# Optimization experiments

Hardware: AMD Instinct MI355X
Metric: run time of the kernel (lower is better)

The kernel has to match this reference:

```python
import jax, jax.numpy as jnp
import numpy as np

B, S, K, N, G = 4, 2048, 4096, 11008, 128  # batch, seq, in_features, out_features, groupsize


def setup_inputs() -> dict:
    key = jax.random.key(0)
    k1, k2, k3, k4 = jax.random.split(key, 4)
    x = jax.random.normal(k1, (B, S, K), dtype=jnp.float32)
    # unpacked int4 codes in [0, 16)
    weight_q = jax.random.randint(k2, (N, K), 0, 16, dtype=jnp.int32)
    # groupwise scales (positive, small) and zeros, packed as [K//G, N, 2]
    scales = jax.random.uniform(k3, (K // G, N), dtype=jnp.float32) * 0.02 + 1e-3
    zeros = jax.random.normal(k4, (K // G, N), dtype=jnp.float32) * 0.1
    scales_and_zeros = jnp.stack([scales, zeros], axis=-1)  # [K//G, N, 2]
    return {"x": x, "weight_q": weight_q, "scales_and_zeros": scales_and_zeros}


def reference(x, weight_q, scales_and_zeros):
    # Dequantize groupwise: w[n,k] = (q[n,k] - 8) * scale[k//G, n] + zero[k//G, n]
    scales = scales_and_zeros[..., 0].T  # [N, K//G]
    zeros = scales_and_zeros[..., 1].T   # [N, K//G]
    q = weight_q.astype(x.dtype).reshape(N, K // G, G)  # [N, K//G, G]
    w = (q - 8.0) * scales[:, :, None] + zeros[:, :, None]  # fused dequant
    w = w.reshape(N, K)
    # y[b,s,n] = sum_k x[b,s,k] * w[n,k]
    return jnp.einsum("bsk,nk->bsn", x, w)
```

## Files before the change

kernel.cpp:

```cpp
#include <hip/hip_runtime.h>
#include <stdint.h>


typedef __attribute__((ext_vector_type(8))) short short8;
typedef __attribute__((ext_vector_type(4))) float float4v;
typedef __attribute__((ext_vector_type(4))) int int4v;
typedef __attribute__((ext_vector_type(2))) float float2v;
typedef __attribute__((ext_vector_type(4))) unsigned short ushort4v;

static constexpr int M_ = 8192;
static constexpr int K_ = 4096;
static constexpr int N_ = 11008;
static constexpr int NKT = K_ / 64;

__device__ __forceinline__ unsigned short f2bf(float f) {
    union { float f; uint32_t u; } v;
    v.f = f;
    uint32_t u = v.u;
    u += 0x7fffu + ((u >> 16) & 1u);
    return (unsigned short)(u >> 16);
}

__device__ __forceinline__ void gload16(const void* g, void* l) {
    __builtin_amdgcn_global_load_lds(
        (const __attribute__((address_space(1))) uint32_t*)g,
        (__attribute__((address_space(3))) uint32_t*)l, 16, 0, 0);
}

__global__ __launch_bounds__(256) void cvt_x_kernel(const float* __restrict__ X,
                                                    unsigned short* __restrict__ Xb) {
    const int i = blockIdx.x * 256 + threadIdx.x;
    const float4v a = ((const float4v*)X)[2 * (size_t)i];
    const float4v b = ((const float4v*)X)[2 * (size_t)i + 1];
    short8 o;
    #pragma unroll
    for (int j = 0; j < 4; ++j) o[j] = (short)f2bf(a[j]);
    #pragma unroll
    for (int j = 0; j < 4; ++j) o[4 + j] = (short)f2bf(b[j]);
    ((short8*)Xb)[(size_t)i] = o;
}

__global__ __launch_bounds__(256) void deq_w_kernel(const int* __restrict__ Q,
                                                    const float* __restrict__ SZ,
                                                    unsigned short* __restrict__ Wb) {
    const int i = blockIdx.x * 256 + threadIdx.x;
    const int n = i >> 9;
    const int c = i & 511;
    const int k0 = c * 8;
    const int g = k0 >> 7;
    const float2v sz = *(const float2v*)(SZ + ((size_t)g * N_ + n) * 2);
    const float s = sz[0], z = sz[1];
    const int4v q0 = *(const int4v*)(Q + (size_t)n * K_ + k0);
    const int4v q1 = *(const int4v*)(Q + (size_t)n * K_ + k0 + 4);
    short8 o;
    #pragma unroll
    for (int j = 0; j < 4; ++j) o[j] = (short)f2bf((float)(q0[j] - 8) * s + z);
    #pragma unroll
    for (int j = 0; j < 4; ++j) o[4 + j] = (short)f2bf((float)(q1[j] - 8) * s + z);
    ((short8*)Wb)[(size_t)i] = o;
}


struct Frags {
    short8 a[4][2];
    short8 b[2][2][2];
};

template <int BUF, int MH>
__device__ __forceinline__ void read_a(const char* ldsB, Frags& f,
                                       int aRB, int k0o, int k1o) {
    const int abase = BUF * 32768 + MH * 16384 + aRB;
    #pragma unroll
    for (int i = 0; i < 4; ++i) {
        f.a[i][0] = *(const short8*)(ldsB + abase + i * 2048 + k0o);
        f.a[i][1] = *(const short8*)(ldsB + abase + i * 2048 + k1o);
    }
}

template <int BUF, int NH>
__device__ __forceinline__ void read_b(const char* ldsB, Frags& f,
                                       int bRB, int k0o, int k1o) {
    const int bbase = 65536 + BUF * 32768 + NH * 16384 + bRB;
    #pragma unroll
    for (int j = 0; j < 2; ++j) {
        f.b[NH][j][0] = *(const short8*)(ldsB + bbase + j * 2048 + k0o);
        f.b[NH][j][1] = *(const short8*)(ldsB + bbase + j * 2048 + k1o);
    }
}

template <int MH, int NH>
__device__ __forceinline__ void phase_mma(Frags& f, float4v (&acc)[8][4]) {
    __builtin_amdgcn_s_setprio(1);
    #pragma unroll
    for (int i = 0; i < 4; ++i)
        #pragma unroll
        for (int j = 0; j < 2; ++j) {
            acc[MH * 4 + i][NH * 2 + j] = __builtin_amdgcn_mfma_f32_16x16x32_bf16(
                f.a[i][0], f.b[NH][j][0], acc[MH * 4 + i][NH * 2 + j], 0, 0, 0);
            acc[MH * 4 + i][NH * 2 + j] = __builtin_amdgcn_mfma_f32_16x16x32_bf16(
                f.a[i][1], f.b[NH][j][1], acc[MH * 4 + i][NH * 2 + j], 0, 0, 0);
        }
    __builtin_amdgcn_s_setprio(0);
}

#define SBAR() __builtin_amdgcn_sched_barrier(0)
#define VMW(n) asm volatile("s_waitcnt vmcnt(" #n ")" ::: "memory")

__global__ __launch_bounds__(512, 2) void gemm_bf16_8ph(
    const unsigned short* __restrict__ Agl,
    const unsigned short* __restrict__ Bgl,
    float* __restrict__ C) {
    __shared__ alignas(16) unsigned short lds[65536];

    const int tid = threadIdx.x;
    const int lane = tid & 63;
    const int wid = tid >> 6;
    const int wr = wid >> 2;
    const int wc = wid & 3;

    const int bid = blockIdx.x;
    const int wg = (bid & 7) * 172 + (bid >> 3);
    const int mt = wg / 43;
    const int nt = wg % 43;
    const int row0 = mt * 256;
    const int col0 = nt * 256;

    const int r8 = lane >> 3;
    const int kc = ((lane & 7) ^ r8) * 8;

    const int l15 = lane & 15;
    const int k0o = ((lane >> 4) * 16) ^ ((l15 & 7) << 4);
    const int k1o = k0o ^ 64;
    const int aRB = (wr * 64 + l15) * 128;
    const int bRB = (wc * 32 + l15) * 128;
    const char* ldsB = (const char*)lds;
    unsigned short* ldsU = lds;

    auto stageA = [&](int kt, int b, int h) {
        #pragma unroll
        for (int i = 0; i < 2; ++i) {
            const int rbase = h * 128 + (wid * 2 + i) * 8;
            gload16(Agl + (size_t)(row0 + rbase + r8) * K_ + kt * 64 + kc,
                    ldsU + b * 16384 + rbase * 64);
        }
    };
    auto stageB = [&](int kt, int b, int h) {
        #pragma unroll
        for (int i = 0; i < 2; ++i) {
            const int rbase = h * 128 + (wid * 2 + i) * 8;
            gload16(Bgl + (size_t)(col0 + rbase + r8) * K_ + kt * 64 + kc,
                    ldsU + 32768 + b * 16384 + rbase * 64);
        }
    };

    float4v acc[8][4] = {};

    stageA(0, 0, 0); stageA(0, 0, 1); stageB(0, 0, 0); stageB(0, 0, 1);
    stageA(1, 1, 0);
    VMW(2);
    __builtin_amdgcn_s_barrier();
    SBAR();

    int t;
#define KTILE(BUF)                                                        \
    {                                                                     \
        Frags f;                                                          \
        read_a<BUF, 0>(ldsB, f, aRB, k0o, k1o);                           \
        read_b<BUF, 0>(ldsB, f, bRB, k0o, k1o);                           \
        if (t + 1 < NKT) { stageA(t + 1, BUF ^ 1, 1); stageB(t + 1, BUF ^ 1, 0); } \
        phase_mma<0, 0>(f, acc);                                          \
        read_b<BUF, 1>(ldsB, f, bRB, k0o, k1o);                           \
        if (t + 1 < NKT) stageB(t + 1, BUF ^ 1, 1);                       \
        phase_mma<0, 1>(f, acc);                                          \
        SBAR();                                                           \
        __builtin_amdgcn_s_barrier();      \
        SBAR();                                                           \
        if (t + 2 < NKT) stageA(t + 2, BUF, 0);                           \
        read_a<BUF, 1>(ldsB, f, aRB, k0o, k1o);                           \
        phase_mma<1, 0>(f, acc);                                          \
        phase_mma<1, 1>(f, acc);                                          \
        SBAR();                                                           \
        if (t + 2 < NKT) { VMW(2); } else { VMW(0); }                     \
        __builtin_amdgcn_s_barrier();       \
        SBAR();                                                           \
    }

    for (int t2 = 0; t2 < NKT; t2 += 2) {
        t = t2;     KTILE(0);
        t = t2 + 1; KTILE(1);
    }
#undef KTILE

    const int lrow = (lane >> 4) * 4;
    #pragma unroll
    for (int mf = 0; mf < 8; ++mf)
        #pragma unroll
        for (int nf = 0; nf < 4; ++nf)
            #pragma unroll
            for (int j = 0; j < 4; ++j) {
                const int r = row0 + (mf >> 2) * 128 + wr * 64 + (mf & 3) * 16 + lrow + j;
                const int c = col0 + (nf >> 1) * 128 + wc * 32 + (nf & 1) * 16 + l15;
                C[(size_t)r * N_ + c] = acc[mf][nf][j];
            }
}

static constexpr int LDSS = 40;

__global__ __launch_bounds__(256, 2) void w4_gemm_fused(
    const float* __restrict__ X, const int* __restrict__ Q,
    const float* __restrict__ SZ, float* __restrict__ C) {
    __shared__ alignas(16) unsigned short As[128 * LDSS];
    __shared__ alignas(16) unsigned short Ws[128 * LDSS];
    const int tid = threadIdx.x;
    const int lane = tid & 63;
    const int wid = tid >> 6;
    const int wrr = wid >> 1;
    const int wcc = wid & 1;
    const int row0 = blockIdx.x * 128;
    const int col0 = blockIdx.y * 128;
    float4v acc[4][4] = {};
    float4v a_reg[4];
    int4v q_reg[4];
    float2v sz_reg[4];

    auto load_tile = [&](int kb) {
        const int g = kb >> 7;
        #pragma unroll
        for (int i = 0; i < 4; ++i) {
            const int idx = tid + 256 * i;
            const int r = idx >> 3;
            const int v = idx & 7;
            a_reg[i] = *(const float4v*)(X + (size_t)(row0 + r) * K_ + kb + v * 4);
            q_reg[i] = *(const int4v*)(Q + (size_t)(col0 + r) * K_ + kb + v * 4);
            sz_reg[i] = *(const float2v*)(SZ + ((size_t)g * N_ + (col0 + r)) * 2);
        }
    };
    auto write_tile = [&]() {
        #pragma unroll
        for (int i = 0; i < 4; ++i) {
            const int idx = tid + 256 * i;
            const int r = idx >> 3;
            const int v = idx & 7;
            ushort4v ab, wb;
            #pragma unroll
            for (int j = 0; j < 4; ++j) ab[j] = f2bf(a_reg[i][j]);
            const float s = sz_reg[i][0];
            const float z = sz_reg[i][1];
            #pragma unroll
            for (int j = 0; j < 4; ++j) wb[j] = f2bf((float)(q_reg[i][j] - 8) * s + z);
            *(ushort4v*)(&As[r * LDSS + v * 4]) = ab;
            *(ushort4v*)(&Ws[r * LDSS + v * 4]) = wb;
        }
    };
    auto compute = [&]() {
        const int lr = lane & 15;
        const int lg = lane >> 4;
        short8 af[4], bf[4];
        #pragma unroll
        for (int mf = 0; mf < 4; ++mf)
            af[mf] = *(const short8*)(&As[(wrr * 64 + mf * 16 + lr) * LDSS + lg * 8]);
        #pragma unroll
        for (int nf = 0; nf < 4; ++nf)
            bf[nf] = *(const short8*)(&Ws[(wcc * 64 + nf * 16 + lr) * LDSS + lg * 8]);
        #pragma unroll
        for (int mf = 0; mf < 4; ++mf)
            #pragma unroll
            for (int nf = 0; nf < 4; ++nf)
                acc[mf][nf] = __builtin_amdgcn_mfma_f32_16x16x32_bf16(
                    af[mf], bf[nf], acc[mf][nf], 0, 0, 0);
    };

    load_tile(0);
    for (int kb = 0; kb < K_; kb += 32) {
        __syncthreads();
        write_tile();
        __syncthreads();
        if (kb + 32 < K_) load_tile(kb + 32);
        compute();
    }
    const int lr = lane & 15;
    const int lg = lane >> 4;
    #pragma unroll
    for (int mf = 0; mf < 4; ++mf)
        #pragma unroll
        for (int nf = 0; nf < 4; ++nf)
            #pragma unroll
            for (int j = 0; j < 4; ++j) {
                const int r = row0 + wrr * 64 + mf * 16 + lg * 4 + j;
                const int c = col0 + wcc * 64 + nf * 16 + lr;
                C[(size_t)r * N_ + c] = acc[mf][nf][j];
            }
}

extern "C" void kernel_launch(void* const* d_in, const int* in_sizes, int n_in,
                              void* d_out, int out_size, void* d_ws, size_t ws_size,
                              hipStream_t stream) {
    const float* X  = (const float*)d_in[0];
    const int*   Q  = (const int*)d_in[1];
    const float* SZ = (const float*)d_in[2];
    float* C = (float*)d_out;

    const size_t xb_bytes = (size_t)M_ * K_ * 2;
    const size_t wb_bytes = (size_t)N_ * K_ * 2;
    if (ws_size >= xb_bytes + wb_bytes) {
        unsigned short* Xb = (unsigned short*)d_ws;
        unsigned short* Wb = (unsigned short*)((char*)d_ws + xb_bytes);
        cvt_x_kernel<<<(M_ * (K_ / 8)) / 256, 256, 0, stream>>>(X, Xb);
        deq_w_kernel<<<(N_ * (K_ / 8)) / 256, 256, 0, stream>>>(Q, SZ, Wb);
        gemm_bf16_8ph<<<dim3(1376), dim3(512), 0, stream>>>(Xb, Wb, C);
    } else {
        dim3 grid(M_ / 128, N_ / 128);
        w4_gemm_fused<<<grid, dim3(256), 0, stream>>>(X, Q, SZ, C);
    }
}
```

Baseline: 744.6 us.

## Software-pipeline LDS fragment reads across k-tiles with double-buffered registers

Splits fragment registers into separate A0/A1 and B0/B1 sets and reorders the four MFMA phases so LDS reads for the next k-tile's first fragments are issued during the current tile's last MFMAs. Barriers and vmcnt waits move to points after the global stages they guard, and the last two tiles are peeled with specialized wait counts. This is meant to hide LDS read latency behind matrix math, at the cost of more live registers, which could cause spills under the 512x2 launch bounds.

Result: slower. 2.183 ms (+193.2%).

```diff
diff --git a/kernel.cpp b/kernel.cpp
--- a/kernel.cpp
+++ b/kernel.cpp
@@ -61,44 +61,40 @@
 }
 
 
-struct Frags {
-    short8 a[4][2];
-    short8 b[2][2][2];
-};
-
 template <int BUF, int MH>
-__device__ __forceinline__ void read_a(const char* ldsB, Frags& f,
+__device__ __forceinline__ void read_a(const char* ldsB, short8 (&a)[4][2],
                                        int aRB, int k0o, int k1o) {
     const int abase = BUF * 32768 + MH * 16384 + aRB;
     #pragma unroll
     for (int i = 0; i < 4; ++i) {
-        f.a[i][0] = *(const short8*)(ldsB + abase + i * 2048 + k0o);
-        f.a[i][1] = *(const short8*)(ldsB + abase + i * 2048 + k1o);
+        a[i][0] = *(const short8*)(ldsB + abase + i * 2048 + k0o);
+        a[i][1] = *(const short8*)(ldsB + abase + i * 2048 + k1o);
     }
 }
 
 template <int BUF, int NH>
-__device__ __forceinline__ void read_b(const char* ldsB, Frags& f,
+__device__ __forceinline__ void read_b(const char* ldsB, short8 (&b)[2][2],
                                        int bRB, int k0o, int k1o) {
     const int bbase = 65536 + BUF * 32768 + NH * 16384 + bRB;
     #pragma unroll
     for (int j = 0; j < 2; ++j) {
-        f.b[NH][j][0] = *(const short8*)(ldsB + bbase + j * 2048 + k0o);
-        f.b[NH][j][1] = *(const short8*)(ldsB + bbase + j * 2048 + k1o);
+        b[j][0] = *(const short8*)(ldsB + bbase + j * 2048 + k0o);
+        b[j][1] = *(const short8*)(ldsB + bbase + j * 2048 + k1o);
     }
 }
 
 template <int MH, int NH>
-__device__ __forceinline__ void phase_mma(Frags& f, float4v (&acc)[8][4]) {
+__device__ __forceinline__ void phase_mma(short8 (&a)[4][2], short8 (&b)[2][2],
+                                          float4v (&acc)[8][4]) {
     __builtin_amdgcn_s_setprio(1);
     #pragma unroll
     for (int i = 0; i < 4; ++i)
         #pragma unroll
         for (int j = 0; j < 2; ++j) {
             acc[MH * 4 + i][NH * 2 + j] = __builtin_amdgcn_mfma_f32_16x16x32_bf16(
-                f.a[i][0], f.b[NH][j][0], acc[MH * 4 + i][NH * 2 + j], 0, 0, 0);
+                a[i][0], b[j][0], acc[MH * 4 + i][NH * 2 + j], 0, 0, 0);
             acc[MH * 4 + i][NH * 2 + j] = __builtin_amdgcn_mfma_f32_16x16x32_bf16(
-                f.a[i][1], f.b[NH][j][1], acc[MH * 4 + i][NH * 2 + j], 0, 0, 0);
+                a[i][1], b[j][1], acc[MH * 4 + i][NH * 2 + j], 0, 0, 0);
         }
     __builtin_amdgcn_s_setprio(0);
 }
@@ -154,41 +150,47 @@
     };
 
     float4v acc[8][4] = {};
+    short8 a0[4][2], a1[4][2];
+    short8 b0[2][2], b1[2][2];
 
     stageA(0, 0, 0); stageA(0, 0, 1); stageB(0, 0, 0); stageB(0, 0, 1);
     stageA(1, 1, 0);
     VMW(2);
     __builtin_amdgcn_s_barrier();
     SBAR();
+    read_a<0, 0>(ldsB, a0, aRB, k0o, k1o);
+    read_b<0, 0>(ldsB, b0, bRB, k0o, k1o);
 
     int t;
-#define KTILE(BUF)                                                        \
-    {                                                                     \
-        Frags f;                                                          \
-        read_a<BUF, 0>(ldsB, f, aRB, k0o, k1o);                           \
-        read_b<BUF, 0>(ldsB, f, bRB, k0o, k1o);                           \
-        if (t + 1 < NKT) { stageA(t + 1, BUF ^ 1, 1); stageB(t + 1, BUF ^ 1, 0); } \
-        phase_mma<0, 0>(f, acc);                                          \
-        read_b<BUF, 1>(ldsB, f, bRB, k0o, k1o);                           \
-        if (t + 1 < NKT) stageB(t + 1, BUF ^ 1, 1);                       \
-        phase_mma<0, 1>(f, acc);                                          \
-        SBAR();                                                           \
-        __builtin_amdgcn_s_barrier();      \
-        SBAR();                                                           \
-        if (t + 2 < NKT) stageA(t + 2, BUF, 0);                           \
-        read_a<BUF, 1>(ldsB, f, aRB, k0o, k1o);                           \
-        phase_mma<1, 0>(f, acc);                                          \
-        phase_mma<1, 1>(f, acc);                                          \
-        SBAR();                                                           \
-        if (t + 2 < NKT) { VMW(2); } else { VMW(0); }                     \
-        __builtin_amdgcn_s_barrier();       \
-        SBAR();                                                           \
-    }
-
-    for (int t2 = 0; t2 < NKT; t2 += 2) {
-        t = t2;     KTILE(0);
-        t = t2 + 1; KTILE(1);
-    }
+#define KTILE(BUF, DN, DN2, MIDW, ENDW)                                    \
+    {                                                                      \
+        read_a<BUF, 1>(ldsB, a1, aRB, k0o, k1o);                           \
+        if (DN) { stageA(t + 1, (BUF) ^ 1, 1); stageB(t + 1, (BUF) ^ 1, 0); } \
+        phase_mma<0, 0>(a0, b0, acc);                                      \
+        read_b<BUF, 1>(ldsB, b1, bRB, k0o, k1o);                           \
+        if (DN) stageB(t + 1, (BUF) ^ 1, 1);                               \
+        phase_mma<1, 0>(a1, b0, acc);                                      \
+        if (DN2) stageA(t + 2, BUF, 0);                                    \
+        if (DN) {                                                          \
+            SBAR(); VMW(MIDW);                                             \
+            __builtin_amdgcn_s_barrier(); SBAR();                          \
+            read_b<(BUF) ^ 1, 0>(ldsB, b0, bRB, k0o, k1o);                 \
+        }                                                                  \
+        phase_mma<0, 1>(a0, b1, acc);                                      \
+        if (DN) read_a<(BUF) ^ 1, 0>(ldsB, a0, aRB, k0o, k1o);             \
+        phase_mma<1, 1>(a1, b1, acc);                                      \
+        if (DN) {                                                          \
+            SBAR(); VMW(ENDW);                                             \
+            __builtin_amdgcn_s_barrier(); SBAR();                          \
+        }                                                                  \
+    }
+
+    for (int t2 = 0; t2 < NKT - 2; t2 += 2) {
+        t = t2;     KTILE(0, 1, 1, 4, 2);
+        t = t2 + 1; KTILE(1, 1, 1, 4, 2);
+    }
+    t = NKT - 2; KTILE(0, 1, 0, 2, 0);
+    t = NKT - 1; KTILE(1, 0, 0, 0, 0);
 #undef KTILE
 
     const int lrow = (lane >> 4) * 4;
```
